# Kernel optimization log

Hardware: AMD Instinct MI355X
Metric: run time of the kernel (lower is better)

Reference implementation:

```python
import jax, jax.numpy as jnp
import numpy as np

B, T, D, H = 4, 2048, 1024, 16
HD = D // H  # 64


def setup_inputs() -> dict:
    key = jax.random.key(0)
    ks = jax.random.split(key, 9)
    s = 1.0 / np.sqrt(D)
    return {
        "x": jax.random.normal(ks[0], (B, T, D), dtype=jnp.float32),
        "Wq": jax.random.uniform(ks[1], (D, D), jnp.float32, -s, s),
        "bq": jax.random.uniform(ks[2], (D,), jnp.float32, -s, s),
        "Wk": jax.random.uniform(ks[3], (D, D), jnp.float32, -s, s),
        "bk": jax.random.uniform(ks[4], (D,), jnp.float32, -s, s),
        "Wv": jax.random.uniform(ks[5], (D, D), jnp.float32, -s, s),
        "bv": jax.random.uniform(ks[6], (D,), jnp.float32, -s, s),
        "Wp": jax.random.uniform(ks[7], (D, D), jnp.float32, -s, s),
        "bp": jax.random.uniform(ks[8], (D,), jnp.float32, -s, s),
    }


def reference(x, Wq, bq, Wk, bk, Wv, bv, Wp, bp):
    b, t, _ = x.shape
    # project and split heads: (B, H, T, HD)
    def heads(w, bias):
        y = x @ w + bias
        return y.reshape(b, t, H, HD).transpose(0, 2, 1, 3)
    q = heads(Wq, bq)
    k = heads(Wk, bk)
    v = heads(Wv, bv)
    scores = jnp.einsum('bhqd,bhkd->bhqk', q, k) / np.sqrt(HD)
    causal = jnp.tril(jnp.ones((t, t), dtype=bool))
    scores = jnp.where(causal, scores, -jnp.inf)
    attn = jax.nn.softmax(scores, axis=-1)  # dropout p=0 -> identity
    out = jnp.einsum('bhqk,bhkd->bhqd', attn, v)
    out = out.transpose(0, 2, 1, 3).reshape(b, t, D)
    return out @ Wp + bp
```

## Files before the change

kernel.cpp:

```cpp
#include <hip/hip_runtime.h>
#include <hip/hip_bf16.h>
#include <stdint.h>

#define B_ 4
#define T_ 2048
#define D_ 1024
#define H_ 16
#define HD_ 64
#define M_TOT (B_ * T_)

typedef unsigned short u16t;
typedef __bf16 bf16x4 __attribute__((ext_vector_type(4)));
typedef __bf16 bf16x8 __attribute__((ext_vector_type(8)));
typedef float f32x4 __attribute__((ext_vector_type(4)));
typedef float f32x16 __attribute__((ext_vector_type(16)));

__device__ __forceinline__ u16t f2bf(float f) {
    union { float f; uint32_t u; } x; x.f = f;
    uint32_t r = x.u + 0x7fffu + ((x.u >> 16) & 1u);
    return (u16t)(r >> 16);
}

__device__ __forceinline__ float fexp2(float x) { return __builtin_amdgcn_exp2f(x); }

__device__ __forceinline__ void gload16(const void* g, void* l) {
    __builtin_amdgcn_global_load_lds((const __attribute__((address_space(1))) void*)g,
                                     (__attribute__((address_space(3))) void*)l, 16, 0, 0);
}

__global__ __launch_bounds__(256) void prep_kernel(const float* __restrict__ x,
                                                   const float* __restrict__ W0,
                                                   const float* __restrict__ W1,
                                                   const float* __restrict__ W2,
                                                   const float* __restrict__ W3,
                                                   u16t* __restrict__ xb,
                                                   u16t* __restrict__ T0,
                                                   u16t* __restrict__ T1,
                                                   u16t* __restrict__ T2,
                                                   u16t* __restrict__ T3) {
    __shared__ u16t tile[64][65];
    const int z = blockIdx.z;
    const int t = threadIdx.x;
    if (z >= 4) {
        int bid = (z - 4) * 256 + blockIdx.y * 16 + blockIdx.x;
        int i = bid * 256 + t;
        const float4* p = (const float4*)x + (size_t)i * 2;
        float4 a = p[0], b = p[1];
        u16t o[8] = {f2bf(a.x), f2bf(a.y), f2bf(a.z), f2bf(a.w),
                     f2bf(b.x), f2bf(b.y), f2bf(b.z), f2bf(b.w)};
        *(uint4*)(xb + (size_t)i * 8) = *(const uint4*)o;
        return;
    }
    const float* W; u16t* To;
    switch (z) {
        case 0: W = W0; To = T0; break;
        case 1: W = W1; To = T1; break;
        case 2: W = W2; To = T2; break;
        default: W = W3; To = T3; break;
    }
    int n0 = blockIdx.x * 64, k0 = blockIdx.y * 64;
#pragma unroll
    for (int i = 0; i < 16; ++i) {
        int idx = i * 256 + t;
        int r = idx >> 6, c = idx & 63;
        tile[r][c] = f2bf(W[(size_t)(k0 + r) * D_ + n0 + c]);
    }
    __syncthreads();
#pragma unroll
    for (int i = 0; i < 16; ++i) {
        int idx = i * 256 + t;
        int r = idx >> 6, c = idx & 63;
        To[(size_t)(n0 + r) * D_ + k0 + c] = tile[c][r];
    }
}

__global__ __launch_bounds__(256) void gemm_qkv_kernel(const u16t* __restrict__ A,
                                                       const u16t* __restrict__ Wt3,
                                                       const float* __restrict__ bq,
                                                       const float* __restrict__ bk,
                                                       const float* __restrict__ bv,
                                                       u16t* __restrict__ qo,
                                                       u16t* __restrict__ ko,
                                                       u16t* __restrict__ vto,
                                                       float qscale) {
    __shared__ u16t smem[32768];
    const int t = threadIdx.x;
    const int lane = t & 63, w = t >> 6;
    const int wm = w >> 1, wn = w & 1;
    const int l15 = lane & 15, l4 = lane >> 4;
    const int m0 = blockIdx.x * 128;
    const int n0g = blockIdx.y * 128;

    const int sr = t >> 3, sc8 = t & 7;
    const int sg = (sc8 ^ (sr & 7)) * 8;

    auto stageg = [&](int k0, int bufoff) {
#pragma unroll
        for (int i = 0; i < 4; ++i) {
            int r = (i * 256 + t) >> 3;
            int ldsoff = bufoff + (i * 256 + w * 64) * 8;
            gload16(&A[(size_t)(m0 + r) * D_ + k0 + sg], &smem[ldsoff]);
            gload16(&Wt3[(size_t)(n0g + r) * D_ + k0 + sg], &smem[16384 + ldsoff]);
        }
    };

    f32x4 acc[4][4] = {};

    auto compute = [&](int bufoff) {
#pragma unroll
        for (int ks = 0; ks < 64; ks += 32) {
            bf16x8 af[4], bf[4];
#pragma unroll
            for (int i = 0; i < 4; ++i) {
                int row = i * 16 + l15;
                int g = (((ks >> 3) + l4) ^ (l15 & 7)) * 8;
                af[i] = *(const bf16x8*)&smem[bufoff + (wm * 64 + row) * 64 + g];
                bf[i] = *(const bf16x8*)&smem[16384 + bufoff + (wn * 64 + row) * 64 + g];
            }
#pragma unroll
            for (int mi = 0; mi < 4; ++mi)
#pragma unroll
                for (int ni = 0; ni < 4; ++ni)
                    acc[mi][ni] = __builtin_amdgcn_mfma_f32_16x16x32_bf16(
                        af[mi], bf[ni], acc[mi][ni], 0, 0, 0);
        }
    };

    stageg(0, 0);
    for (int kk = 0; kk < 16; kk += 2) {
        __syncthreads();
        stageg((kk + 1) * 64, 8192);
        compute(0);
        __syncthreads();
        if (kk + 2 < 16) stageg((kk + 2) * 64, 0);
        compute(8192);
    }

    const int sel = blockIdx.y >> 3;
    const int n0 = (blockIdx.y & 7) * 128;
    const float* bias = sel == 0 ? bq : (sel == 1 ? bk : bv);
    const float scale = sel == 0 ? qscale : 1.0f;

#pragma unroll
    for (int mi = 0; mi < 4; ++mi) {
#pragma unroll
        for (int ni = 0; ni < 4; ++ni) {
            int col = n0 + wn * 64 + ni * 16 + l15;
            float bn = bias[col];
            if (sel < 2) {
                u16t* outp = sel == 0 ? qo : ko;
#pragma unroll
                for (int r = 0; r < 4; ++r) {
                    int row = m0 + wm * 64 + mi * 16 + l4 * 4 + r;
                    outp[(size_t)row * D_ + col] = f2bf((acc[mi][ni][r] + bn) * scale);
                }
            } else {
                int token0 = m0 + wm * 64 + mi * 16 + l4 * 4;
                u16t o4[4];
#pragma unroll
                for (int r = 0; r < 4; ++r) o4[r] = f2bf(acc[mi][ni][r] + bn);
                int b = token0 >> 11, tb = token0 & (T_ - 1);
                int h = col >> 6, hd = col & 63;
                *(uint2*)&vto[(((size_t)b * H_ + h) * HD_ + hd) * T_ + tb] = *(const uint2*)o4;
            }
        }
    }
}

__global__ __launch_bounds__(256) void gemm_proj_kernel(const u16t* __restrict__ A,
                                                        const u16t* __restrict__ Wt,
                                                        const float* __restrict__ bias,
                                                        float* __restrict__ outp) {
    __shared__ u16t smem[32768];
    const int t = threadIdx.x;
    const int lane = t & 63, w = t >> 6;
    const int wm = w >> 1, wn = w & 1;
    const int l15 = lane & 15, l4 = lane >> 4;
    const int m0 = blockIdx.x * 128, n0 = blockIdx.y * 128;

    const int sr = t >> 3, sc8 = t & 7;
    const int sg = (sc8 ^ (sr & 7)) * 8;

    auto stageg = [&](int k0, int bufoff) {
#pragma unroll
        for (int i = 0; i < 4; ++i) {
            int r = (i * 256 + t) >> 3;
            int ldsoff = bufoff + (i * 256 + w * 64) * 8;
            gload16(&A[(size_t)(m0 + r) * D_ + k0 + sg], &smem[ldsoff]);
            gload16(&Wt[(size_t)(n0 + r) * D_ + k0 + sg], &smem[16384 + ldsoff]);
        }
    };

    f32x4 acc[4][4] = {};

    auto compute = [&](int bufoff) {
#pragma unroll
        for (int ks = 0; ks < 64; ks += 32) {
            bf16x8 af[4], bf[4];
#pragma unroll
            for (int i = 0; i < 4; ++i) {
                int row = i * 16 + l15;
                int g = (((ks >> 3) + l4) ^ (l15 & 7)) * 8;
                af[i] = *(const bf16x8*)&smem[bufoff + (wm * 64 + row) * 64 + g];
                bf[i] = *(const bf16x8*)&smem[16384 + bufoff + (wn * 64 + row) * 64 + g];
            }
#pragma unroll
            for (int mi = 0; mi < 4; ++mi)
#pragma unroll
                for (int ni = 0; ni < 4; ++ni)
                    acc[mi][ni] = __builtin_amdgcn_mfma_f32_16x16x32_bf16(
                        af[mi], bf[ni], acc[mi][ni], 0, 0, 0);
        }
    };

    stageg(0, 0);
    for (int kk = 0; kk < 16; kk += 2) {
        __syncthreads();
        stageg((kk + 1) * 64, 8192);
        compute(0);
        __syncthreads();
        if (kk + 2 < 16) stageg((kk + 2) * 64, 0);
        compute(8192);
    }

#pragma unroll
    for (int mi = 0; mi < 4; ++mi) {
#pragma unroll
        for (int ni = 0; ni < 4; ++ni) {
            int col = n0 + wn * 64 + ni * 16 + l15;
            float bn = bias[col];
#pragma unroll
            for (int r = 0; r < 4; ++r) {
                int row = m0 + wm * 64 + mi * 16 + l4 * 4 + r;
                outp[(size_t)row * D_ + col] = acc[mi][ni][r] + bn;
            }
        }
    }
}

__global__ __launch_bounds__(256) void attn_kernel(const u16t* __restrict__ Q,
                                                   const u16t* __restrict__ K,
                                                   const u16t* __restrict__ Vt,
                                                   u16t* __restrict__ O) {
    __shared__ u16t smem[16384];

    const int t = threadIdx.x;
    const int lane = t & 63, w = t >> 6;
    const int l31 = lane & 31, l5 = lane >> 5;

    const int lin = blockIdx.x;
    const int bh = lin & 63;
    const int q_idx = lin >> 6;
    const int hi = q_idx >> 2, lo = q_idx & 3;
    const int qtile = ((0x348F >> (hi * 4)) & 15) ^ ((0x2130 >> (lo * 4)) & 15);

    const size_t base = (size_t)(bh >> 4) * T_ * D_ + (size_t)(bh & 15) * HD_;
    const size_t vtbase = (size_t)bh * HD_ * T_;
    const int q0 = qtile * 128;
    const int qsub0 = q0 + w * 32;
    const int sw = l31 & 7;

    const int sr = t >> 3, sc16 = t & 7;
    const int g16 = sc16 ^ (sr & 7);
    const u16t* kp = &K[base + (size_t)sr * D_ + g16 * 8];
    const u16t* vp = &Vt[vtbase + (size_t)sr * T_ + g16 * 8];

    auto stage = [&](int jt, int buf) {
        const u16t* kq = kp + (size_t)jt * 64 * D_;
        const u16t* vq = vp + (size_t)jt * 64;
        u16t* kd = smem + buf * 4096;
        u16t* vd = smem + 8192 + buf * 4096;
#pragma unroll
        for (int c = 0; c < 2; ++c) {
            gload16(kq + (size_t)c * 32 * D_, kd + c * 2048 + w * 512);
            gload16(vq + (size_t)c * 32 * T_, vd + c * 2048 + w * 512);
        }
    };

    const u16t* qp = &Q[base + (size_t)(qsub0 + l31) * D_ + l5 * 8];
    bf16x8 qf[4];
#pragma unroll
    for (int ks = 0; ks < 4; ++ks) qf[ks] = *(const bf16x8*)&qp[ks * 16];

    f32x16 acc_oT[2] = {};
    float lrun = 0.f;

    const int njt = 2 * qtile + 2;
    stage(0, 0);

    for (int jt = 0; jt < njt; ++jt) {
        const int cur = jt & 1;
        const int kv0 = jt * 64;
        __syncthreads();
        if (jt + 1 < njt) stage(jt + 1, cur ^ 1);

        if (kv0 <= qsub0 + 31) {
            const u16t* kb = smem + cur * 4096;
            const u16t* vb = smem + 8192 + cur * 4096;

            f32x16 accs[2] = {};
            __builtin_amdgcn_s_setprio(1);
#pragma unroll
            for (int half = 0; half < 2; ++half) {
                const u16t* kr = kb + (half * 32 + l31) * 64;
#pragma unroll
                for (int ks = 0; ks < 4; ++ks) {
                    bf16x8 kf = *(const bf16x8*)&kr[((ks * 2 + l5) ^ sw) * 8];
                    accs[half] = __builtin_amdgcn_mfma_f32_32x32x16_bf16(
                        kf, qf[ks], accs[half], 0, 0, 0);
                }
            }
            __builtin_amdgcn_s_setprio(0);

            const int qrow = qsub0 + l31;
            if (kv0 + 63 > qsub0) {
#pragma unroll
                for (int half = 0; half < 2; ++half)
#pragma unroll
                    for (int r = 0; r < 16; ++r) {
                        int kv = kv0 + half * 32 + (r & 3) + 8 * (r >> 2) + 4 * l5;
                        if (kv > qrow) accs[half][r] = -1e30f;
                    }
            }

            float ps[4] = {0.f, 0.f, 0.f, 0.f};
            bf16x8 pb[4];
#pragma unroll
            for (int half = 0; half < 2; ++half)
#pragma unroll
                for (int r = 0; r < 16; ++r) {
                    float p = fexp2(accs[half][r]);
                    ps[r & 3] += p;
                    pb[half * 2 + (r >> 3)][r & 7] = (__bf16)p;
                }
            lrun += (ps[0] + ps[1]) + (ps[2] + ps[3]);

            __builtin_amdgcn_s_setprio(1);
#pragma unroll
            for (int dh = 0; dh < 2; ++dh) {
                const u16t* vr = vb + (dh * 32 + l31) * 64;
#pragma unroll
                for (int m = 0; m < 4; ++m) {
                    int g = 2 * (m & 1) + 4 * (m >> 1);
                    bf16x4 v0 = *(const bf16x4*)&vr[((g ^ sw) << 3) + 4 * l5];
                    bf16x4 v1 = *(const bf16x4*)&vr[(((g + 1) ^ sw) << 3) + 4 * l5];
                    bf16x8 af = __builtin_shufflevector(v0, v1, 0, 1, 2, 3, 4, 5, 6, 7);
                    acc_oT[dh] = __builtin_amdgcn_mfma_f32_32x32x16_bf16(
                        af, pb[m], acc_oT[dh], 0, 0, 0);
                }
            }
            __builtin_amdgcn_s_setprio(0);
        }
    }

    lrun += __shfl_xor(lrun, 32);
    __syncthreads();
    float inv = __builtin_amdgcn_rcpf(lrun);
    u16t* ot = smem + w * 2304;
#pragma unroll
    for (int dh = 0; dh < 2; ++dh)
#pragma unroll
        for (int r = 0; r < 16; ++r) {
            int d = dh * 32 + (r & 3) + 8 * (r >> 2) + 4 * l5;
            ot[l31 * 72 + d] = f2bf(acc_oT[dh][r] * inv);
        }
    __syncthreads();
#pragma unroll
    for (int p = 0; p < 4; ++p) {
        int idx = p * 64 + lane;
        int row = idx >> 3, c8 = (idx & 7) * 8;
        *(uint4*)&O[base + (size_t)(qsub0 + row) * D_ + c8] = *(const uint4*)&ot[row * 72 + c8];
    }
}

extern "C" void kernel_launch(void* const* d_in, const int* in_sizes, int n_in,
                              void* d_out, int out_size, void* d_ws, size_t ws_size,
                              hipStream_t stream) {
    const float* x  = (const float*)d_in[0];
    const float* Wq = (const float*)d_in[1];
    const float* bq = (const float*)d_in[2];
    const float* Wk = (const float*)d_in[3];
    const float* bk = (const float*)d_in[4];
    const float* Wv = (const float*)d_in[5];
    const float* bv = (const float*)d_in[6];
    const float* Wp = (const float*)d_in[7];
    const float* bp = (const float*)d_in[8];
    float* out = (float*)d_out;

    u16t* ws = (u16t*)d_ws;
    const size_t XN = (size_t)M_TOT * D_;
    u16t* xb  = ws;
    u16t* q   = ws + XN;
    u16t* k   = ws + 2 * XN;
    u16t* vt  = ws + 3 * XN;
    u16t* wtq = ws + 4 * XN;
    u16t* wtk = wtq + (size_t)D_ * D_;
    u16t* wtv = wtk + (size_t)D_ * D_;
    u16t* wtp = wtv + (size_t)D_ * D_;
    u16t* o   = xb;

    prep_kernel<<<dim3(16, 16, 20), 256, 0, stream>>>(x, Wq, Wk, Wv, Wp,
                                                      xb, wtq, wtk, wtv, wtp);

    gemm_qkv_kernel<<<dim3(64, 24), 256, 0, stream>>>(
        xb, wtq, bq, bk, bv, q, k, vt, 0.125f * 1.44269504088896f);

    attn_kernel<<<dim3(1024), 256, 0, stream>>>(q, k, vt, o);

    gemm_proj_kernel<<<dim3(64, 8), 256, 0, stream>>>(o, wtp, bp, out);
}
```

Measured before the change: 151.7 us.

## Triple-buffer QKV GEMM with K=32 stages and explicit vmcnt waits

Restructures the QKV projection GEMM main loop from a double-buffered 64-wide K tile to a triple-buffered 32-wide K tile pipeline. Global-to-LDS loads are issued two stages ahead, and explicit s_waitcnt vmcnt plus raw barriers with sched_barrier fences control ordering. Precomputed LDS offsets and a new 4-chunk XOR swizzle replace per-iteration address math. The aim is to hide global load latency better and cut LDS use. The cost is more barriers per unit of K and fragile hand-written wait counts.

```diff
diff --git a/kernel.cpp b/kernel.cpp
--- a/kernel.cpp
+++ b/kernel.cpp
@@ -83,7 +83,7 @@
                                                        u16t* __restrict__ ko,
                                                        u16t* __restrict__ vto,
                                                        float qscale) {
-    __shared__ u16t smem[32768];
+    __shared__ u16t smem[24576];
     const int t = threadIdx.x;
     const int lane = t & 63, w = t >> 6;
     const int wm = w >> 1, wn = w & 1;
@@ -91,50 +91,68 @@
     const int m0 = blockIdx.x * 128;
     const int n0g = blockIdx.y * 128;
 
-    const int sr = t >> 3, sc8 = t & 7;
-    const int sg = (sc8 ^ (sr & 7)) * 8;
-
-    auto stageg = [&](int k0, int bufoff) {
+    const int sr2 = t >> 2;
+    const int gsw = ((t & 3) ^ ((sr2 >> 1) & 3)) * 8;
+    const u16t* pA = &A[(size_t)(m0 + sr2) * D_ + gsw];
+    const u16t* pB = &Wt3[(size_t)(n0g + sr2) * D_ + gsw];
+    int kof = 0;
+
+    auto stage = [&](int bnoff) {
+        gload16(pA + kof,         smem + bnoff + w * 512);
+        gload16(pA + 65536 + kof, smem + bnoff + 2048 + w * 512);
+        gload16(pB + kof,         smem + 12288 + bnoff + w * 512);
+        gload16(pB + 65536 + kof, smem + 12288 + bnoff + 2048 + w * 512);
+        kof += 32;
+    };
+
+    const int gr = ((l4 ^ ((l15 >> 1) & 3)) << 3);
+    int aoff[4], boff[4];
+#pragma unroll
+    for (int i = 0; i < 4; ++i) {
+        aoff[i] = (wm * 64 + i * 16 + l15) * 32 + gr;
+        boff[i] = (wn * 64 + i * 16 + l15) * 32 + gr;
+    }
+
+    f32x4 acc[4][4] = {};
+
+    auto compute = [&](int bcoff) {
+        bf16x8 af[4], bf[4];
 #pragma unroll
         for (int i = 0; i < 4; ++i) {
-            int r = (i * 256 + t) >> 3;
-            int ldsoff = bufoff + (i * 256 + w * 64) * 8;
-            gload16(&A[(size_t)(m0 + r) * D_ + k0 + sg], &smem[ldsoff]);
-            gload16(&Wt3[(size_t)(n0g + r) * D_ + k0 + sg], &smem[16384 + ldsoff]);
-        }
-    };
-
-    f32x4 acc[4][4] = {};
-
-    auto compute = [&](int bufoff) {
-#pragma unroll
-        for (int ks = 0; ks < 64; ks += 32) {
-            bf16x8 af[4], bf[4];
-#pragma unroll
-            for (int i = 0; i < 4; ++i) {
-                int row = i * 16 + l15;
-                int g = (((ks >> 3) + l4) ^ (l15 & 7)) * 8;
-                af[i] = *(const bf16x8*)&smem[bufoff + (wm * 64 + row) * 64 + g];
-                bf[i] = *(const bf16x8*)&smem[16384 + bufoff + (wn * 64 + row) * 64 + g];
-            }
-#pragma unroll
-            for (int mi = 0; mi < 4; ++mi)
-#pragma unroll
-                for (int ni = 0; ni < 4; ++ni)
-                    acc[mi][ni] = __builtin_amdgcn_mfma_f32_16x16x32_bf16(
-                        af[mi], bf[ni], acc[mi][ni], 0, 0, 0);
-        }
-    };
-
-    stageg(0, 0);
-    for (int kk = 0; kk < 16; kk += 2) {
-        __syncthreads();
-        stageg((kk + 1) * 64, 8192);
-        compute(0);
-        __syncthreads();
-        if (kk + 2 < 16) stageg((kk + 2) * 64, 0);
-        compute(8192);
-    }
+            af[i] = *(const bf16x8*)&smem[bcoff + aoff[i]];
+            bf[i] = *(const bf16x8*)&smem[12288 + bcoff + boff[i]];
+        }
+#pragma unroll
+        for (int mi = 0; mi < 4; ++mi)
+#pragma unroll
+            for (int ni = 0; ni < 4; ++ni)
+                acc[mi][ni] = __builtin_amdgcn_mfma_f32_16x16x32_bf16(
+                    af[mi], bf[ni], acc[mi][ni], 0, 0, 0);
+    };
+
+    auto iter = [&](int bcoff, int bnoff, int vm, bool dostage) {
+        asm volatile("s_waitcnt lgkmcnt(0)" ::: "memory");
+        __builtin_amdgcn_s_barrier();
+        __builtin_amdgcn_sched_barrier(0);
+        if (dostage) stage(bnoff);
+        __builtin_amdgcn_sched_barrier(0);
+        if (vm == 8)      asm volatile("s_waitcnt vmcnt(8)" ::: "memory");
+        else if (vm == 4) asm volatile("s_waitcnt vmcnt(4)" ::: "memory");
+        else              asm volatile("s_waitcnt vmcnt(0)" ::: "memory");
+        __builtin_amdgcn_sched_barrier(0);
+        __builtin_amdgcn_s_barrier();
+        compute(bcoff);
+    };
+
+    stage(0);
+    stage(4096);
+    for (int tt = 0; tt < 30; tt += 3) {
+        iter(0, 8192, 8, true);
+        iter(4096, 0, 8, true);
+        iter(8192, 4096, 8, true);
+    }
+    iter(0, 8192, 4, false);
+    iter(4096, 0, 0, false);
 
     const int sel = blockIdx.y >> 3;
     const int n0 = (blockIdx.y & 7) * 128;
```

New measurement: 151.7 us. No clear change (-0.0%).

## Enlarge QKV GEMM tile to 256x256 with 8-wave phased pipeline

Applied to the files above, without the earlier changes.

The QKV projection GEMM moves from a 128x128 tile with 4 waves to a 256x256 tile with 8 waves, using 128KB of dynamic LDS for two K-stage buffers. The main loop is split into eight phases per two K-steps. Each phase interleaves LDS fragment reads, global-to-LDS prefetch issues, explicit barriers and waitcnt, and MFMA bursts raised with s_setprio. The goal is more data reuse per loaded byte and better overlap of loads with MFMA work. The cost is a grid of only 384 blocks, which risks lower occupancy and poor CU balance.

```diff
diff --git a/kernel.cpp b/kernel.cpp
--- a/kernel.cpp
+++ b/kernel.cpp
@@ -74,7 +74,7 @@
     }
 }
 
-__global__ __launch_bounds__(256) void gemm_qkv_kernel(const u16t* __restrict__ A,
+__global__ __launch_bounds__(512) void gemm_qkv_kernel(const u16t* __restrict__ A,
                                                        const u16t* __restrict__ Wt3,
                                                        const float* __restrict__ bq,
                                                        const float* __restrict__ bk,
@@ -83,79 +83,119 @@
                                                        u16t* __restrict__ ko,
                                                        u16t* __restrict__ vto,
                                                        float qscale) {
-    __shared__ u16t smem[32768];
+    extern __shared__ u16t smem[];
     const int t = threadIdx.x;
     const int lane = t & 63, w = t >> 6;
-    const int wm = w >> 1, wn = w & 1;
+    const int wm = w >> 2, wn = w & 3;
     const int l15 = lane & 15, l4 = lane >> 4;
-    const int m0 = blockIdx.x * 128;
-    const int n0g = blockIdx.y * 128;
-
-    const int sr = t >> 3, sc8 = t & 7;
-    const int sg = (sc8 ^ (sr & 7)) * 8;
-
-    auto stageg = [&](int k0, int bufoff) {
-#pragma unroll
-        for (int i = 0; i < 4; ++i) {
-            int r = (i * 256 + t) >> 3;
-            int ldsoff = bufoff + (i * 256 + w * 64) * 8;
-            gload16(&A[(size_t)(m0 + r) * D_ + k0 + sg], &smem[ldsoff]);
-            gload16(&Wt3[(size_t)(n0g + r) * D_ + k0 + sg], &smem[16384 + ldsoff]);
-        }
-    };
-
-    f32x4 acc[4][4] = {};
-
-    auto compute = [&](int bufoff) {
-#pragma unroll
-        for (int ks = 0; ks < 64; ks += 32) {
-            bf16x8 af[4], bf[4];
-#pragma unroll
-            for (int i = 0; i < 4; ++i) {
-                int row = i * 16 + l15;
-                int g = (((ks >> 3) + l4) ^ (l15 & 7)) * 8;
-                af[i] = *(const bf16x8*)&smem[bufoff + (wm * 64 + row) * 64 + g];
-                bf[i] = *(const bf16x8*)&smem[16384 + bufoff + (wn * 64 + row) * 64 + g];
-            }
-#pragma unroll
-            for (int mi = 0; mi < 4; ++mi)
-#pragma unroll
-                for (int ni = 0; ni < 4; ++ni)
-                    acc[mi][ni] = __builtin_amdgcn_mfma_f32_16x16x32_bf16(
-                        af[mi], bf[ni], acc[mi][ni], 0, 0, 0);
-        }
-    };
-
-    stageg(0, 0);
-    for (int kk = 0; kk < 16; kk += 2) {
-        __syncthreads();
-        stageg((kk + 1) * 64, 8192);
-        compute(0);
-        __syncthreads();
-        if (kk + 2 < 16) stageg((kk + 2) * 64, 0);
-        compute(8192);
-    }
-
-    const int sel = blockIdx.y >> 3;
-    const int n0 = (blockIdx.y & 7) * 128;
+    const int m0 = blockIdx.x * 256;
+    const int ny = blockIdx.y;
+
+    const int sr = t >> 3;
+    const int sg = ((t & 7) ^ (sr & 7)) * 8;
+    const u16t* Ag = A + (size_t)(m0 + sr) * D_ + sg;
+    const u16t* Bg = Wt3 + (size_t)(ny * 256 + sr) * D_ + sg;
+
+    auto issA = [&](int b, int h, int q, int kof) {
+        gload16(Ag + (size_t)(h * 128 + q * 64) * D_ + kof,
+                smem + b * 16384 + h * 8192 + q * 4096 + w * 512);
+    };
+    auto issB = [&](int b, int h, int q, int kof) {
+        gload16(Bg + (size_t)(h * 128 + q * 64) * D_ + kof,
+                smem + 32768 + b * 16384 + h * 8192 + q * 4096 + w * 512);
+    };
+
+    const int gk0 = (l4 ^ (l15 & 7)) * 8;
+    const int gk1 = ((4 + l4) ^ (l15 & 7)) * 8;
+    const int arow = wm * 8192 + l15 * 64;
+    const int brow = (wn >> 1) * 8192 + ((wn & 1) * 64 + l15) * 64;
+
+    f32x4 acc[8][4] = {};
+    bf16x8 bfr[4][2];
+    bf16x8 afr[2][2];
+
+    auto rdq = [&](int Ab, int Bb, int p) {
+        if (p == 0) {
+#pragma unroll
+            for (int ni = 0; ni < 4; ++ni) {
+                bfr[ni][0] = *(const bf16x8*)&smem[Bb + brow + ni * 1024 + gk0];
+                bfr[ni][1] = *(const bf16x8*)&smem[Bb + brow + ni * 1024 + gk1];
+            }
+        }
+#pragma unroll
+        for (int ri = 0; ri < 2; ++ri) {
+            afr[ri][0] = *(const bf16x8*)&smem[Ab + arow + p * 2048 + ri * 1024 + gk0];
+            afr[ri][1] = *(const bf16x8*)&smem[Ab + arow + p * 2048 + ri * 1024 + gk1];
+        }
+    };
+    auto mmaq = [&](int p) {
+#pragma unroll
+        for (int ri = 0; ri < 2; ++ri)
+#pragma unroll
+            for (int ni = 0; ni < 4; ++ni) {
+                acc[p * 2 + ri][ni] = __builtin_amdgcn_mfma_f32_16x16x32_bf16(
+                    afr[ri][0], bfr[ni][0], acc[p * 2 + ri][ni], 0, 0, 0);
+                acc[p * 2 + ri][ni] = __builtin_amdgcn_mfma_f32_16x16x32_bf16(
+                    afr[ri][1], bfr[ni][1], acc[p * 2 + ri][ni], 0, 0, 0);
+            }
+    };
+
+#define PH(Ab, Bb, P, ISS, TAIL)                                   \
+    rdq(Ab, Bb, P);                                                \
+    ISS;                                                           \
+    __builtin_amdgcn_s_barrier();                                  \
+    asm volatile("s_waitcnt lgkmcnt(0)" ::: "memory");             \
+    __builtin_amdgcn_sched_barrier(0);                             \
+    __builtin_amdgcn_s_setprio(1);                                 \
+    mmaq(P);                                                       \
+    __builtin_amdgcn_s_setprio(0);                                 \
+    TAIL;                                                          \
+    __builtin_amdgcn_s_barrier();
+
+    issB(0, 0, 0, 0);  issB(0, 0, 1, 0);  issB(0, 1, 0, 0);  issB(0, 1, 1, 0);
+    issA(0, 0, 0, 0);  issA(0, 1, 0, 0);  issA(0, 0, 1, 0);  issA(0, 1, 1, 0);
+    issB(1, 0, 0, 64); issB(1, 0, 1, 64); issB(1, 1, 0, 64); issB(1, 1, 1, 64);
+    issA(1, 0, 0, 64); issA(1, 1, 0, 64);
+    asm volatile("s_waitcnt vmcnt(6)" ::: "memory");
+    __builtin_amdgcn_s_barrier();
+
+    for (int i = 0; i < 8; ++i) {
+        const bool nl = i < 7;
+        const int kp1 = i * 128 + 64, kn0 = i * 128 + 128, kn1 = i * 128 + 192;
+        PH(0, 32768, 0, { issA(1, 0, 1, kp1); issA(1, 1, 1, kp1); }, {})
+        PH(0, 32768, 1, { if (nl) { issB(0, 0, 0, kn0); issB(0, 0, 1, kn0); } }, {})
+        PH(0, 32768, 2, { if (nl) { issB(0, 1, 0, kn0); issB(0, 1, 1, kn0); } }, {})
+        PH(0, 32768, 3, { if (nl) { issA(0, 0, 0, kn0); issA(0, 1, 0, kn0); } },
+                        { if (nl) { asm volatile("s_waitcnt vmcnt(6)" ::: "memory"); }
+                          else    { asm volatile("s_waitcnt vmcnt(0)" ::: "memory"); } })
+        PH(16384, 49152, 0, { if (nl) { issA(0, 0, 1, kn0); issA(0, 1, 1, kn0); } }, {})
+        PH(16384, 49152, 1, { if (nl) { issB(1, 0, 0, kn1); issB(1, 0, 1, kn1); } }, {})
+        PH(16384, 49152, 2, { if (nl) { issB(1, 1, 0, kn1); issB(1, 1, 1, kn1); } }, {})
+        PH(16384, 49152, 3, { if (nl) { issA(1, 0, 0, kn1); issA(1, 1, 0, kn1); } },
+                            { if (nl) { asm volatile("s_waitcnt vmcnt(6)" ::: "memory"); } })
+    }
+#undef PH
+
+    const int sel = ny >> 2;
+    const int n0 = (ny & 3) * 256 + wn * 64;
     const float* bias = sel == 0 ? bq : (sel == 1 ? bk : bv);
     const float scale = sel == 0 ? qscale : 1.0f;
 
 #pragma unroll
-    for (int mi = 0; mi < 4; ++mi) {
+    for (int mi = 0; mi < 8; ++mi) {
 #pragma unroll
         for (int ni = 0; ni < 4; ++ni) {
-            int col = n0 + wn * 64 + ni * 16 + l15;
+            int col = n0 + ni * 16 + l15;
             float bn = bias[col];
             if (sel < 2) {
                 u16t* outp = sel == 0 ? qo : ko;
 #pragma unroll
                 for (int r = 0; r < 4; ++r) {
-                    int row = m0 + wm * 64 + mi * 16 + l4 * 4 + r;
+                    int row = m0 + wm * 128 + mi * 16 + l4 * 4 + r;
                     outp[(size_t)row * D_ + col] = f2bf((acc[mi][ni][r] + bn) * scale);
                 }
             } else {
-                int token0 = m0 + wm * 64 + mi * 16 + l4 * 4;
+                int token0 = m0 + wm * 128 + mi * 16 + l4 * 4;
                 u16t o4[4];
 #pragma unroll
                 for (int r = 0; r < 4; ++r) o4[r] = f2bf(acc[mi][ni][r] + bn);
@@ -399,10 +439,13 @@
     u16t* wtp = wtv + (size_t)D_ * D_;
     u16t* o   = xb;
 
+    hipFuncSetAttribute((const void*)gemm_qkv_kernel,
+                        hipFuncAttributeMaxDynamicSharedMemorySize, 131072);
+
     prep_kernel<<<dim3(16, 16, 20), 256, 0, stream>>>(x, Wq, Wk, Wv, Wp,
                                                       xb, wtq, wtk, wtv, wtp);
 
-    gemm_qkv_kernel<<<dim3(64, 24), 256, 0, stream>>>(
+    gemm_qkv_kernel<<<dim3(32, 12), 512, 131072, stream>>>(
         xb, wtq, bq, bk, bv, q, k, vt, 0.125f * 1.44269504088896f);
 
     attn_kernel<<<dim3(1024), 256, 0, stream>>>(q, k, vt, o);
```

Result: no change. 152.7 us (+0.7%).
